# Performance work log

Hardware: AMD Instinct MI355X
Metric: run time of the kernel (lower is better)

The kernel has to match this reference:

```python
import jax, jax.numpy as jnp
import numpy as np

D_IN, D_HID, D_OUT = 4096, 8192, 1000


def setup_inputs() -> dict:
    key = jax.random.key(0)
    ks = jax.random.split(key, 7)
    s1 = 1.0 / np.sqrt(D_IN)
    s2 = 1.0 / np.sqrt(D_HID)
    return {
        "x": jax.random.normal(ks[0], (D_IN,), dtype=jnp.float32),
        "W1": jax.random.normal(ks[1], (D_HID, D_IN), dtype=jnp.float32) * s1,
        "b1": jax.random.normal(ks[2], (D_HID,), dtype=jnp.float32) * 0.01,
        "W2": jax.random.normal(ks[3], (D_HID, D_HID), dtype=jnp.float32) * s2,
        "b2": jax.random.normal(ks[4], (D_HID,), dtype=jnp.float32) * 0.01,
        "W3": jax.random.normal(ks[5], (D_OUT, D_HID), dtype=jnp.float32) * s2,
        "b3": jax.random.normal(ks[6], (D_OUT,), dtype=jnp.float32) * 0.01,
    }


def reference(x, W1, b1, W2, b2, W3, b3):
    # layer 1: matvec + bias + square activation (h_relu is x*x)
    h = W1 @ x + b1
    h = h * h
    # layer 2
    h = W2 @ h + b2
    h = h * h
    # layer 3 (no activation)
    return W3 @ h + b3
```

## Files before the change

kernel.cpp:

```cpp
#include <hip/hip_runtime.h>
#include <hip/hip_bf16.h>


template<int K>
__global__ __launch_bounds__(256) void matvec2row(
    const float* __restrict__ W,
    const float* __restrict__ x,
    const float* __restrict__ bias,
    float* __restrict__ y,
    int do_square)
{
    constexpr int K4   = K / 4;
    constexpr int ITER = K4 / 256;
    const int row0 = blockIdx.x * 2;
    const int tid  = threadIdx.x;

    const float4* __restrict__ Wa = (const float4*)(W + (size_t)row0 * K);
    const float4* __restrict__ Wb = (const float4*)(W + (size_t)(row0 + 1) * K);
    const float4* __restrict__ x4 = (const float4*)x;

    float acc0 = 0.0f, acc1 = 0.0f;
    #pragma unroll
    for (int it = 0; it < ITER; ++it) {
        const int i = tid + it * 256;
        float4 v  = x4[i];
        float4 wa = Wa[i];
        float4 wb = Wb[i];
        acc0 += wa.x * v.x + wa.y * v.y + wa.z * v.z + wa.w * v.w;
        acc1 += wb.x * v.x + wb.y * v.y + wb.z * v.z + wb.w * v.w;
    }

    #pragma unroll
    for (int off = 32; off > 0; off >>= 1) {
        acc0 += __shfl_down(acc0, off, 64);
        acc1 += __shfl_down(acc1, off, 64);
    }

    __shared__ float s0[4], s1[4];
    const int wave = tid >> 6;
    if ((tid & 63) == 0) { s0[wave] = acc0; s1[wave] = acc1; }
    __syncthreads();

    if (tid == 0) {
        float r0 = (s0[0] + s0[1]) + (s0[2] + s0[3]);
        float r1 = (s1[0] + s1[1]) + (s1[2] + s1[3]);
        r0 += bias[row0];
        r1 += bias[row0 + 1];
        if (do_square) { r0 = r0 * r0; r1 = r1 * r1; }
        y[row0]     = r0;
        y[row0 + 1] = r1;
    }
}

extern "C" void kernel_launch(void* const* d_in, const int* in_sizes, int n_in,
                              void* d_out, int out_size, void* d_ws, size_t ws_size,
                              hipStream_t stream) {
    const float* x  = (const float*)d_in[0];
    const float* W1 = (const float*)d_in[1];
    const float* b1 = (const float*)d_in[2];
    const float* W2 = (const float*)d_in[3];
    const float* b2 = (const float*)d_in[4];
    const float* W3 = (const float*)d_in[5];
    const float* b3 = (const float*)d_in[6];
    float* out = (float*)d_out;

    const int D_HID = 8192, D_OUT = 1000;

    float* h1 = (float*)d_ws;
    float* h2 = h1 + D_HID;

    matvec2row<4096><<<D_HID / 2, 256, 0, stream>>>(W1, x, b1, h1, 1);
    matvec2row<8192><<<D_HID / 2, 256, 0, stream>>>(W2, h1, b2, h2, 1);
    matvec2row<8192><<<D_OUT / 2, 256, 0, stream>>>(W3, h2, b3, out, 0);
}
```

Measured before the change: 451.7 us.

## Restructure MLP matvecs with shared-memory input, multi-row blocks and atomic accumulation

```diff
diff --git a/kernel.cpp b/kernel.cpp
--- a/kernel.cpp
+++ b/kernel.cpp
@@ -1,54 +1,61 @@
 #include <hip/hip_runtime.h>
-#include <hip/hip_bf16.h>
 
 
-template<int K>
-__global__ __launch_bounds__(256) void matvec2row(
+__global__ __launch_bounds__(256) void init_bias(
+    const float* __restrict__ b1, const float* __restrict__ b2,
+    const float* __restrict__ b3,
+    float* __restrict__ h1, float* __restrict__ h2, float* __restrict__ out)
+{
+    const int i = blockIdx.x * 256 + threadIdx.x;
+    if (i < 8192)       h1[i] = b1[i];
+    else if (i < 16384) h2[i - 8192] = b2[i - 8192];
+    else if (i < 17384) out[i - 16384] = b3[i - 16384];
+}
+
+template<int K, int RPB, int SQ>
+__global__ __launch_bounds__(256) void matvec_atomic(
     const float* __restrict__ W,
-    const float* __restrict__ x,
-    const float* __restrict__ bias,
-    float* __restrict__ y,
-    int do_square)
+    const float* __restrict__ xin,
+    float* __restrict__ y)
 {
-    constexpr int K4   = K / 4;
-    constexpr int ITER = K4 / 256;
-    const int row0 = blockIdx.x * 2;
-    const int tid  = threadIdx.x;
+    constexpr int K4     = K / 4;
+    constexpr int CHUNKS = K4 / 256;
 
-    const float4* __restrict__ Wa = (const float4*)(W + (size_t)row0 * K);
-    const float4* __restrict__ Wb = (const float4*)(W + (size_t)(row0 + 1) * K);
-    const float4* __restrict__ x4 = (const float4*)x;
+    __shared__ __align__(16) float sx[K];
+    const int tid = threadIdx.x;
 
-    float acc0 = 0.0f, acc1 = 0.0f;
+    const float4* __restrict__ x4 = (const float4*)xin;
+    float4* sx4 = (float4*)sx;
     #pragma unroll
-    for (int it = 0; it < ITER; ++it) {
-        const int i = tid + it * 256;
-        float4 v  = x4[i];
-        float4 wa = Wa[i];
-        float4 wb = Wb[i];
-        acc0 += wa.x * v.x + wa.y * v.y + wa.z * v.z + wa.w * v.w;
-        acc1 += wb.x * v.x + wb.y * v.y + wb.z * v.z + wb.w * v.w;
+    for (int c = 0; c < CHUNKS; ++c) {
+        const int i = c * 256 + tid;
+        float4 v = x4[i];
+        if (SQ) { v.x *= v.x; v.y *= v.y; v.z *= v.z; v.w *= v.w; }
+        sx4[i] = v;
     }
-
-    #pragma unroll
-    for (int off = 32; off > 0; off >>= 1) {
-        acc0 += __shfl_down(acc0, off, 64);
-        acc1 += __shfl_down(acc1, off, 64);
-    }
-
-    __shared__ float s0[4], s1[4];
-    const int wave = tid >> 6;
-    if ((tid & 63) == 0) { s0[wave] = acc0; s1[wave] = acc1; }
     __syncthreads();
 
-    if (tid == 0) {
-        float r0 = (s0[0] + s0[1]) + (s0[2] + s0[3]);
-        float r1 = (s1[0] + s1[1]) + (s1[2] + s1[3]);
-        r0 += bias[row0];
-        r1 += bias[row0 + 1];
-        if (do_square) { r0 = r0 * r0; r1 = r1 * r1; }
-        y[row0]     = r0;
-        y[row0 + 1] = r1;
+    const int  c0   = blockIdx.x % CHUNKS;
+    const long row0 = (long)blockIdx.x * RPB;
+
+    for (int r = 0; r < RPB; ++r) {
+        const long row = row0 + r;
+        const float4* __restrict__ Wr = (const float4*)(W + row * (long)K);
+
+        float acc = 0.0f;
+        #pragma unroll
+        for (int j = 0; j < CHUNKS; ++j) {
+            int c = c0 + j; if (c >= CHUNKS) c -= CHUNKS;
+            const int i = c * 256 + tid;
+            const float4 w = Wr[i];
+            const float4 v = sx4[i];
+            acc += (w.x * v.x + w.y * v.y) + (w.z * v.z + w.w * v.w);
+        }
+
+        #pragma unroll
+        for (int off = 32; off > 0; off >>= 1)
+            acc += __shfl_down(acc, off, 64);
+        if ((tid & 63) == 0) atomicAdd(&y[row], acc);
     }
 }
 
@@ -64,12 +71,12 @@
     const float* b3 = (const float*)d_in[6];
     float* out = (float*)d_out;
 
-    const int D_HID = 8192, D_OUT = 1000;
+    float* h1 = (float*)d_ws;
+    float* h2 = h1 + 8192;
 
-    float* h1 = (float*)d_ws;
-    float* h2 = h1 + D_HID;
+    init_bias<<<68, 256, 0, stream>>>(b1, b2, b3, h1, h2, out);
 
-    matvec2row<4096><<<D_HID / 2, 256, 0, stream>>>(W1, x, b1, h1, 1);
-    matvec2row<8192><<<D_HID / 2, 256, 0, stream>>>(W2, h1, b2, h2, 1);
-    matvec2row<8192><<<D_OUT / 2, 256, 0, stream>>>(W3, h2, b3, out, 0);
+    matvec_atomic<4096, 8, 0><<<1024, 256, 0, stream>>>(W1, x, h1);
+    matvec_atomic<8192, 8, 1><<<1024, 256, 0, stream>>>(W2, h1, h2);
+    matvec_atomic<8192, 2, 1><<<500, 256, 0, stream>>>(W3, h2, out);
 }
```

Result: slower. 467.7 us (+3.5%).
